# Kernel tuning notes

Measured on AMD Instinct MI355X. Metric: run time of the kernel, lower is better.

The kernel has to match this reference:

```python
import jax, jax.numpy as jnp
import numpy as np

N = 500_000        # num nodes
E = 2_000_000      # num edges
D = 8              # message passing depth
DIM = 16           # dim_embed
F = 5              # NUM_NODE_FEATURES
NUM_DAGS = 5_000


def _mlp_params(key, d_in, d_out, scale=0.1):
    k1, k2, k3 = jax.random.split(key, 3)
    return (jax.random.normal(k1, (d_in, 16), jnp.float32) * scale, jnp.zeros((16,), jnp.float32),
            jax.random.normal(k2, (16, 8), jnp.float32) * scale, jnp.zeros((8,), jnp.float32),
            jax.random.normal(k3, (8, d_out), jnp.float32) * scale, jnp.zeros((d_out,), jnp.float32))


def _mlp(x, w1, b1, w2, b2, w3, b3):
    h = jax.nn.relu(x @ w1 + b1)
    h = jax.nn.relu(h @ w2 + b2)
    return h @ w3 + b3


def setup_inputs() -> dict:
    key = jax.random.key(0)
    ks = jax.random.split(key, 8)
    x = jax.random.normal(ks[0], (N, F), jnp.float32)
    edge_index = jax.random.randint(ks[1], (2, E), 0, N, jnp.int32)
    edge_mask_batch = jax.random.bernoulli(ks[2], 0.5, (D, E))
    ptr = jnp.arange(0, N + 1, N // NUM_DAGS, dtype=jnp.int32)  # 5000 dags of 100 nodes
    inp = {"x": x, "edge_index": edge_index, "edge_mask_batch": edge_mask_batch, "ptr": ptr}
    names = ["p", "m", "u", "d", "g"]
    dins = [F, DIM, DIM, F + DIM, DIM]
    for name, din, k in zip(names, dins, jax.random.split(ks[3], 5)):
        w1, b1, w2, b2, w3, b3 = _mlp_params(k, din, DIM)
        inp.update({f"{name}w1": w1, f"{name}b1": b1, f"{name}w2": w2,
                    f"{name}b2": b2, f"{name}w3": w3, f"{name}b3": b3})
    return inp


def reference(x, edge_index, edge_mask_batch, ptr,
              pw1, pb1, pw2, pb2, pw3, pb3,
              mw1, mb1, mw2, mb2, mw3, mb3,
              uw1, ub1, uw2, ub2, uw3, ub3,
              dw1, db1, dw2, db2, dw3, db3,
              gw1, gb1, gw2, gb2, gw3, gb3):
    num_nodes = x.shape[0]
    dst, src = edge_index[0], edge_index[1]

    # NodeEncoder: prep then D rounds of masked sparse message passing
    h = _mlp(x, pw1, pb1, pw2, pb2, pw3, pb3)  # [N, DIM]

    def step(h, mask):
        mf = mask.astype(h.dtype)  # [E]
        y = _mlp(h, mw1, mb1, mw2, mb2, mw3, mb3)  # [N, DIM]
        # adj @ y: out[i] = sum over active edges (i <- j) of y[j]
        agg = jnp.zeros_like(h).at[dst].add(y[src] * mf[:, None])
        # node_mask: nodes that are destinations of an active edge
        nm = (jnp.zeros((num_nodes,), h.dtype).at[dst].add(mf) > 0)
        upd = _mlp(agg, uw1, ub1, uw2, ub2, uw3, ub3)
        return h + nm[:, None].astype(h.dtype) * upd, None

    h, _ = jax.lax.scan(step, h, edge_mask_batch)
    node_embeddings = h

    # DagEncoder: per-dag segment-sum of mlp([x, h])
    num_dags = ptr.shape[0] - 1
    seg = jnp.searchsorted(ptr, jnp.arange(num_nodes, dtype=ptr.dtype), side='right') - 1
    z = _mlp(jnp.concatenate([x, node_embeddings], axis=1), dw1, db1, dw2, db2, dw3, db3)
    dag_summaries = jax.ops.segment_sum(z, seg, num_segments=num_dags)  # [num_dags, DIM]

    # GlobalEncoder: no obs_ptr -> sum over all dags
    g = _mlp(dag_summaries, gw1, gb1, gw2, gb2, gw3, gb3)
    global_summaries = g.sum(0)[None]  # [1, DIM]

    return node_embeddings, dag_summaries, global_summaries
```

## Files before the change

kernel.cpp:

```cpp
#include <hip/hip_runtime.h>
#include <hip/hip_bf16.h>
#include <stdint.h>

#define N_NODES 500000
#define HALF_N 250000
#define N_EDGES 2000000
#define DEPTH 8
#define NUM_DAGS 5000
#define DAG_SZ 100
#define OUT_NODES_ELEMS 8000000
#define OUT_GLOB_OFF    8080000

#define EPB 1024
#define NB_E 1954
#define NBUK 256
#define NBUK_USED 245
#define MHIST (NBUK * NB_E)
#define NB_SCAN2 489

typedef __hip_bfloat16 bf16;

__device__ __forceinline__ float bfb2f(unsigned u) {
    return __uint_as_float((u & 0xffffu) << 16);
}
__device__ __forceinline__ unsigned f2bfb(float f) {
    bf16 b = __float2bfloat16(f);
    unsigned short u;
    __builtin_memcpy(&u, &b, 2);
    return (unsigned)u;
}
__device__ __forceinline__ float rndbf(float f) { return bfb2f(f2bfb(f)); }
template<int ISBF>
__device__ __forceinline__ float crnd(float f) { return ISBF ? rndbf(f) : f; }

__device__ __forceinline__ void unpack_pair(uint4 a, uint4 b, float* f) {
    f[0]=bfb2f(a.x);  f[1]=bfb2f(a.x>>16);
    f[2]=bfb2f(a.y);  f[3]=bfb2f(a.y>>16);
    f[4]=bfb2f(a.z);  f[5]=bfb2f(a.z>>16);
    f[6]=bfb2f(a.w);  f[7]=bfb2f(a.w>>16);
    f[8]=bfb2f(b.x);  f[9]=bfb2f(b.x>>16);
    f[10]=bfb2f(b.y); f[11]=bfb2f(b.y>>16);
    f[12]=bfb2f(b.z); f[13]=bfb2f(b.z>>16);
    f[14]=bfb2f(b.w); f[15]=bfb2f(b.w>>16);
}
__device__ __forceinline__ unsigned packpair(float lo, float hi) {
    return f2bfb(lo) | (f2bfb(hi) << 16);
}
__device__ __forceinline__ void pack16(const float* f, uint4* a, uint4* b) {
    a->x = packpair(f[0],f[1]);   a->y = packpair(f[2],f[3]);
    a->z = packpair(f[4],f[5]);   a->w = packpair(f[6],f[7]);
    b->x = packpair(f[8],f[9]);   b->y = packpair(f[10],f[11]);
    b->z = packpair(f[12],f[13]); b->w = packpair(f[14],f[15]);
}

template<int ISBF>
__device__ __forceinline__ float ldf(const void* p, size_t i) {
    return ISBF ? __bfloat162float(((const bf16*)p)[i]) : ((const float*)p)[i];
}
template<int ISBF>
__device__ __forceinline__ void load16(const void* base, size_t row, float* f) {
    if (ISBF) {
        const uint4* p = (const uint4*)((const bf16*)base + row*16);
        uint4 a = p[0], b = p[1];
        unpack_pair(a, b, f);
    } else {
        const float4* p = (const float4*)((const float*)base + row*16);
        float4 v0=p[0], v1=p[1], v2=p[2], v3=p[3];
        f[0]=v0.x; f[1]=v0.y; f[2]=v0.z; f[3]=v0.w;
        f[4]=v1.x; f[5]=v1.y; f[6]=v1.z; f[7]=v1.w;
        f[8]=v2.x; f[9]=v2.y; f[10]=v2.z; f[11]=v2.w;
        f[12]=v3.x; f[13]=v3.y; f[14]=v3.z; f[15]=v3.w;
    }
}
template<int ISBF>
__device__ __forceinline__ void store16(void* base, size_t row, const float* f) {
    if (ISBF) {
        uint4 a, b; pack16(f, &a, &b);
        uint4* p = (uint4*)((bf16*)base + row*16);
        p[0] = a; p[1] = b;
    } else {
        float4* p = (float4*)((float*)base + row*16);
        p[0] = make_float4(f[0],f[1],f[2],f[3]);
        p[1] = make_float4(f[4],f[5],f[6],f[7]);
        p[2] = make_float4(f[8],f[9],f[10],f[11]);
        p[3] = make_float4(f[12],f[13],f[14],f[15]);
    }
}

__global__ void k_detect(const void* __restrict__ x, int* __restrict__ flag) {
    const unsigned short* u = (const unsigned short*)x;
    int t = threadIdx.x;
    int wild = 0;
    #pragma unroll
    for (int k = 0; k < 4; k++) {
        float v = bfb2f(u[t*4 + k]);
        if (fabsf(v) > 1000.f) wild = 1;
    }
    unsigned long long m = __ballot(wild);
    if (t == 0) flag[0] = (m == 0ull) ? 1 : 0;
}

template<int DIN, int ISBF>
__device__ __forceinline__ void load_mlp_smem(const void* w1, const void* b1,
        const void* w2, const void* b2, const void* w3, const void* b3,
        float* s) {
    const int n1 = DIN * 16;
    const int tot = n1 + 16 + 128 + 8 + 128 + 16;
    for (int i = threadIdx.x; i < tot; i += blockDim.x) {
        int o = i; float v;
        if (o < n1)                 v = ldf<ISBF>(w1, o);
        else if ((o -= n1) < 16)    v = ldf<ISBF>(b1, o);
        else if ((o -= 16) < 128)   v = ldf<ISBF>(w2, o);
        else if ((o -= 128) < 8)    v = ldf<ISBF>(b2, o);
        else if ((o -= 8) < 128)    v = ldf<ISBF>(w3, o);
        else                        v = ldf<ISBF>(b3, o - 128);
        s[i] = v;
    }
}

template<int DIN, int ISBF>
__device__ __forceinline__ void mlp_apply(const float* in, const float* s,
                                          float* out) {
    const float* w1 = s;
    const float* b1 = s + DIN * 16;
    const float* w2 = b1 + 16;
    const float* b2 = w2 + 128;
    const float* w3 = b2 + 8;
    const float* b3 = w3 + 128;
    float h1[16];
    #pragma unroll
    for (int j = 0; j < 16; j++) {
        float a = b1[j];
        #pragma unroll
        for (int i = 0; i < DIN; i++) a = fmaf(in[i], w1[i*16 + j], a);
        h1[j] = crnd<ISBF>(fmaxf(a, 0.f));
    }
    float h2[8];
    #pragma unroll
    for (int j = 0; j < 8; j++) {
        float a = b2[j];
        #pragma unroll
        for (int i = 0; i < 16; i++) a = fmaf(h1[i], w2[i*8 + j], a);
        h2[j] = crnd<ISBF>(fmaxf(a, 0.f));
    }
    #pragma unroll
    for (int j = 0; j < 16; j++) {
        float a = b3[j];
        #pragma unroll
        for (int i = 0; i < 8; i++) a = fmaf(h2[i], w3[i*16 + j], a);
        out[j] = crnd<ISBF>(a);
    }
}


__global__ __launch_bounds__(256)
void k_bhist(const int* __restrict__ dstp, int* __restrict__ bh) {
    __shared__ int hcnt[NBUK];
    int t = threadIdx.x, blk = blockIdx.x;
    hcnt[t] = 0;
    __syncthreads();
    #pragma unroll
    for (int k = 0; k < 4; k++) {
        int e = blk * EPB + k * 256 + t;
        if (e < N_EDGES) atomicAdd(&hcnt[dstp[e] >> 11], 1);
    }
    __syncthreads();
    bh[t * NB_E + blk] = hcnt[t];
}

__global__ __launch_bounds__(256)
void k_gbsum(const int* __restrict__ v, int n, int* __restrict__ bsum) {
    __shared__ int sd[256];
    int b = blockIdx.x, t = threadIdx.x;
    int base = b * 1024;
    int s = 0;
    #pragma unroll
    for (int k = 0; k < 4; k++) {
        int i = base + t + k * 256;
        if (i < n) s += v[i];
    }
    sd[t] = s; __syncthreads();
    for (int off = 128; off > 0; off >>= 1) {
        if (t < off) sd[t] += sd[t + off];
        __syncthreads();
    }
    if (t == 0) bsum[b] = sd[0];
}

__global__ __launch_bounds__(512)
void k_gbscan(const int* __restrict__ bsum, int nb, int* __restrict__ boff) {
    __shared__ int s[512];
    int t = threadIdx.x;
    int v = (t < nb) ? bsum[t] : 0;
    s[t] = v; __syncthreads();
    for (int off = 1; off < 512; off <<= 1) {
        int x = (t >= off) ? s[t - off] : 0;
        __syncthreads();
        s[t] += x;
        __syncthreads();
    }
    if (t < nb) boff[t] = s[t] - v;
}

__global__ __launch_bounds__(1024)
void k_gscan(const int* __restrict__ v, const int* __restrict__ boff, int n,
             int* __restrict__ out) {
    __shared__ int s[1024];
    int b = blockIdx.x, t = threadIdx.x;
    int i = b * 1024 + t;
    int x = (i < n) ? v[i] : 0;
    s[t] = x; __syncthreads();
    for (int off = 1; off < 1024; off <<= 1) {
        int y = (t >= off) ? s[t - off] : 0;
        __syncthreads();
        s[t] += y;
        __syncthreads();
    }
    if (i < n) out[i] = boff[b] + s[t] - x;
}

__global__ __launch_bounds__(256)
void k_bscatter(const int* __restrict__ dstp, const int* __restrict__ srcp,
                const int* __restrict__ mask, const int* __restrict__ sbh,
                uint2* __restrict__ staging) {
    __shared__ int cur[NBUK];
    int t = threadIdx.x, blk = blockIdx.x;
    cur[t] = sbh[t * NB_E + blk];
    __syncthreads();
    #pragma unroll
    for (int k = 0; k < 4; k++) {
        int e = blk * EPB + k * 256 + t;
        if (e < N_EDGES) {
            int d = dstp[e];
            unsigned mb = 0;
            #pragma unroll
            for (int tt = 0; tt < DEPTH; tt++)
                mb |= (__builtin_nontemporal_load(mask + (size_t)tt * N_EDGES + e)
                       != 0 ? 1u : 0u) << tt;
            int pos = atomicAdd(&cur[d >> 11], 1);
            staging[pos] = make_uint2((unsigned)srcp[e] | (mb << 19), (unsigned)d);
        }
    }
}

__global__ __launch_bounds__(256)
void k_place(const uint2* __restrict__ staging, const int* __restrict__ sbh,
             int* __restrict__ row_ptr, unsigned* __restrict__ csr) {
    __shared__ int cnt[2048];
    __shared__ int tsum[256];
    int t = threadIdx.x, b = blockIdx.x;
    int ebase = sbh[b * NB_E];
    int eend  = sbh[(b + 1) * NB_E];
    int nrec  = eend - ebase;
    #pragma unroll
    for (int k = 0; k < 8; k++) cnt[t + k * 256] = 0;
    __syncthreads();
    for (int r = t; r < nrec; r += 256)
        atomicAdd(&cnt[staging[ebase + r].y & 2047], 1);
    __syncthreads();
    int s = 0;
    #pragma unroll
    for (int j = 0; j < 8; j++) { int c = cnt[t*8 + j]; cnt[t*8 + j] = s; s += c; }
    int own = s;
    tsum[t] = s;
    __syncthreads();
    for (int off = 1; off < 256; off <<= 1) {
        int v = (t >= off) ? tsum[t - off] : 0;
        __syncthreads();
        tsum[t] += v;
        __syncthreads();
    }
    int pref = tsum[t] - own + ebase;
    #pragma unroll
    for (int j = 0; j < 8; j++) cnt[t*8 + j] += pref;
    int base_node = b * 2048;
    #pragma unroll
    for (int j = 0; j < 8; j++) {
        int idx = base_node + t*8 + j;
        if (idx <= N_NODES) row_ptr[idx] = cnt[t*8 + j];
    }
    __syncthreads();
    for (int r = t; r < nrec; r += 256) {
        uint2 u = staging[ebase + r];
        int pos = atomicAdd(&cnt[u.y & 2047], 1);
        csr[pos] = u.x;
    }
}


template<int ISBF>
__device__ __forceinline__ void prep_body(const void* x,
        const void* pw1, const void* pb1, const void* pw2,
        const void* pb2, const void* pw3, const void* pb3,
        const void* mw1, const void* mb1, const void* mw2,
        const void* mb2, const void* mw3, const void* mb3,
        void* h, bf16* y0, float* sp, float* sm) {
    load_mlp_smem<5, ISBF>(pw1, pb1, pw2, pb2, pw3, pb3, sp);
    load_mlp_smem<16, ISBF>(mw1, mb1, mw2, mb2, mw3, mb3, sm);
    __syncthreads();
    int i = blockIdx.x * blockDim.x + threadIdx.x;
    if (i >= N_NODES) return;
    float in[5];
    #pragma unroll
    for (int j = 0; j < 5; j++) in[j] = ldf<ISBF>(x, (size_t)i*5 + j);
    float hv[16];
    mlp_apply<5, ISBF>(in, sp, hv);
    store16<ISBF>(h, i, hv);
    float y[16];
    mlp_apply<16, ISBF>(hv, sm, y);
    uint4 oa, ob; pack16(y, &oa, &ob);
    uint4* yp = (uint4*)(y0 + (size_t)i*16);
    yp[0] = oa; yp[1] = ob;
}

__global__ __launch_bounds__(256, 4)
void k_prep(const void* __restrict__ x,
            const void* pw1, const void* pb1, const void* pw2,
            const void* pb2, const void* pw3, const void* pb3,
            const void* mw1, const void* mb1, const void* mw2,
            const void* mb2, const void* mw3, const void* mb3,
            void* __restrict__ h, bf16* __restrict__ y0,
            const int* __restrict__ dtflag) {
    __shared__ float sp[5*16 + 16 + 128 + 8 + 128 + 16];
    __shared__ float sm[16*16 + 16 + 128 + 8 + 128 + 16];
    if (dtflag[0])
        prep_body<1>(x, pw1,pb1,pw2,pb2,pw3,pb3, mw1,mb1,mw2,mb2,mw3,mb3, h, y0, sp, sm);
    else
        prep_body<0>(x, pw1,pb1,pw2,pb2,pw3,pb3, mw1,mb1,mw2,mb2,mw3,mb3, h, y0, sp, sm);
}

template<int ISBF>
__device__ __forceinline__ void finish_node(int i, int any, const float* acc,
        void* h, const bf16* yin, bf16* yout, const float* su, const float* sm) {
    uint4* yo = (uint4*)(yout + (size_t)i*16);
    if (!any) {
        const uint4* yp = (const uint4*)(yin + (size_t)i*16);
        yo[0] = yp[0]; yo[1] = yp[1];
        return;
    }
    float a16[16];
    #pragma unroll
    for (int j = 0; j < 16; j++) a16[j] = crnd<ISBF>(acc[j]);
    float upd[16];
    mlp_apply<16, ISBF>(a16, su, upd);
    float hv[16];
    load16<ISBF>(h, i, hv);
    float o[16];
    #pragma unroll
    for (int j = 0; j < 16; j++) o[j] = crnd<ISBF>(hv[j] + upd[j]);
    store16<ISBF>(h, i, o);
    float yn[16];
    mlp_apply<16, ISBF>(o, sm, yn);
    uint4 oa, ob; pack16(yn, &oa, &ob);
    yo[0] = oa; yo[1] = ob;
}

template<int ISBF>
__device__ __forceinline__ void round_body(void* h, const int* row_ptr,
        const unsigned* csr, const bf16* yin, bf16* yout,
        const void* uw1, const void* ub1, const void* uw2,
        const void* ub2, const void* uw3, const void* ub3,
        const void* mw1, const void* mb1, const void* mw2,
        const void* mb2, const void* mw3, const void* mb3,
        int t, float* su, float* sm) {
    load_mlp_smem<16, ISBF>(uw1, ub1, uw2, ub2, uw3, ub3, su);
    load_mlp_smem<16, ISBF>(mw1, mb1, mw2, mb2, mw3, mb3, sm);
    __syncthreads();
    int i0 = blockIdx.x * blockDim.x + threadIdx.x;
    if (i0 >= HALF_N) return;
    int i1 = i0 + HALF_N;
    int b0 = row_ptr[i0], e0 = row_ptr[i0 + 1];
    int b1 = row_ptr[i1], e1 = row_ptr[i1 + 1];
    float acc0[16], acc1[16];
    #pragma unroll
    for (int j = 0; j < 16; j++) { acc0[j] = 0.f; acc1[j] = 0.f; }
    int any0 = 0, any1 = 0;
    const unsigned tb = 1u << (19 + t);
    int p0 = b0, p1 = b1;
    while (p0 < e0 || p1 < e1) {
        unsigned v0[4], v1[4];
        #pragma unroll
        for (int k = 0; k < 4; k++) {
            v0[k] = (p0 + k < e0) ? csr[p0 + k] : 0u;
            v1[k] = (p1 + k < e1) ? csr[p1 + k] : 0u;
        }
        uint4 ga0[4], gb0[4], ga1[4], gb1[4];
        int a0[4], a1[4];
        #pragma unroll
        for (int k = 0; k < 4; k++) {
            a0[k] = (v0[k] & tb) != 0;
            if (a0[k]) {
                const uint4* yp = (const uint4*)(yin + (size_t)(v0[k] & 0x7FFFF)*16);
                ga0[k] = yp[0]; gb0[k] = yp[1];
            }
            a1[k] = (v1[k] & tb) != 0;
            if (a1[k]) {
                const uint4* yp = (const uint4*)(yin + (size_t)(v1[k] & 0x7FFFF)*16);
                ga1[k] = yp[0]; gb1[k] = yp[1];
            }
        }
        #pragma unroll
        for (int k = 0; k < 4; k++) {
            if (a0[k]) {
                any0 = 1;
                float f[16]; unpack_pair(ga0[k], gb0[k], f);
                #pragma unroll
                for (int j = 0; j < 16; j++) acc0[j] += f[j];
            }
            if (a1[k]) {
                any1 = 1;
                float f[16]; unpack_pair(ga1[k], gb1[k], f);
                #pragma unroll
                for (int j = 0; j < 16; j++) acc1[j] += f[j];
            }
        }
        p0 += 4; p1 += 4;
    }
    finish_node<ISBF>(i0, any0, acc0, h, yin, yout, su, sm);
    finish_node<ISBF>(i1, any1, acc1, h, yin, yout, su, sm);
}

__global__ __launch_bounds__(256, 4)
void k_round(void* __restrict__ h, const int* __restrict__ row_ptr,
             const unsigned* __restrict__ csr,
             const bf16* __restrict__ yin, bf16* __restrict__ yout,
             const void* uw1, const void* ub1, const void* uw2,
             const void* ub2, const void* uw3, const void* ub3,
             const void* mw1, const void* mb1, const void* mw2,
             const void* mb2, const void* mw3, const void* mb3,
             int t, const int* __restrict__ dtflag) {
    __shared__ float su[16*16 + 16 + 128 + 8 + 128 + 16];
    __shared__ float sm[16*16 + 16 + 128 + 8 + 128 + 16];
    if (dtflag[0])
        round_body<1>(h, row_ptr, csr, yin, yout, uw1,ub1,uw2,ub2,uw3,ub3,
                      mw1,mb1,mw2,mb2,mw3,mb3, t, su, sm);
    else
        round_body<0>(h, row_ptr, csr, yin, yout, uw1,ub1,uw2,ub2,uw3,ub3,
                      mw1,mb1,mw2,mb2,mw3,mb3, t, su, sm);
}

template<int ISBF>
__device__ __forceinline__ void dag_body(const void* x, const void* h,
        const void* w1, const void* b1, const void* w2,
        const void* b2, const void* w3, const void* b3,
        float* dagsum, float* s, float* zb) {
    load_mlp_smem<21, ISBF>(w1, b1, w2, b2, w3, b3, s);
    __syncthreads();
    int t = threadIdx.x;
    int dag = blockIdx.x;
    if (t < DAG_SZ) {
        int i = dag * DAG_SZ + t;
        float in[21];
        #pragma unroll
        for (int j = 0; j < 5; j++) in[j] = ldf<ISBF>(x, (size_t)i*5 + j);
        load16<ISBF>(h, i, in + 5);
        float z[16];
        mlp_apply<21, ISBF>(in, s, z);
        #pragma unroll
        for (int j = 0; j < 16; j++) zb[t*16 + j] = z[j];
    }
    __syncthreads();
    if (t < 16) {
        float acc = 0.f;
        for (int r = 0; r < DAG_SZ; r++) acc += zb[r*16 + t];
        dagsum[(size_t)dag*16 + t] = acc;
    }
}

__global__ __launch_bounds__(128)
void k_dag(const void* __restrict__ x, const void* __restrict__ h,
           const void* w1, const void* b1, const void* w2,
           const void* b2, const void* w3, const void* b3,
           float* __restrict__ dagsum, const int* __restrict__ dtflag) {
    __shared__ float s[21*16 + 16 + 128 + 8 + 128 + 16];
    __shared__ float zb[DAG_SZ * 16];
    if (dtflag[0]) dag_body<1>(x, h, w1,b1,w2,b2,w3,b3, dagsum, s, zb);
    else           dag_body<0>(x, h, w1,b1,w2,b2,w3,b3, dagsum, s, zb);
}

template<int ISBF>
__device__ __forceinline__ void glob_body(const float* dagsum,
        const void* w1, const void* b1, const void* w2,
        const void* b2, const void* w3, const void* b3,
        void* d_out, float* globacc, float* s, float* gb) {
    load_mlp_smem<16, ISBF>(w1, b1, w2, b2, w3, b3, s);
    __syncthreads();
    int t = threadIdx.x;
    int d = blockIdx.x * blockDim.x + t;
    float g[16];
    if (d < NUM_DAGS) {
        const float4* dp = (const float4*)(dagsum + (size_t)d*16);
        float4 v0 = dp[0], v1 = dp[1], v2 = dp[2], v3 = dp[3];
        float in[16] = { v0.x, v0.y, v0.z, v0.w, v1.x, v1.y, v1.z, v1.w,
                         v2.x, v2.y, v2.z, v2.w, v3.x, v3.y, v3.z, v3.w };
        #pragma unroll
        for (int j = 0; j < 16; j++) in[j] = crnd<ISBF>(in[j]);
        if (ISBF) {
            bf16* od = (bf16*)d_out + OUT_NODES_ELEMS;
            store16<1>(od, d, in);
        } else {
            float* od = (float*)d_out + OUT_NODES_ELEMS;
            store16<0>(od, d, in);
        }
        mlp_apply<16, ISBF>(in, s, g);
    } else {
        #pragma unroll
        for (int j = 0; j < 16; j++) g[j] = 0.f;
    }
    #pragma unroll
    for (int j = 0; j < 16; j++) gb[t*16 + j] = g[j];
    __syncthreads();
    if (t < 16) {
        float acc = 0.f;
        for (int r = 0; r < 256; r++) acc += gb[r*16 + t];
        unsafeAtomicAdd(&globacc[t], acc);
    }
}

__global__ __launch_bounds__(256)
void k_glob(const float* __restrict__ dagsum,
            const void* w1, const void* b1, const void* w2,
            const void* b2, const void* w3, const void* b3,
            void* __restrict__ d_out, float* __restrict__ globacc,
            const int* __restrict__ dtflag) {
    __shared__ float s[16*16 + 16 + 128 + 8 + 128 + 16];
    __shared__ float gb[256 * 16];
    if (dtflag[0]) glob_body<1>(dagsum, w1,b1,w2,b2,w3,b3, d_out, globacc, s, gb);
    else           glob_body<0>(dagsum, w1,b1,w2,b2,w3,b3, d_out, globacc, s, gb);
}

__global__ void k_final(const float* __restrict__ globacc,
                        void* __restrict__ d_out, const int* __restrict__ dtflag) {
    const int isbf = dtflag[0];
    int t = threadIdx.x;
    if (t < 16) {
        if (isbf) ((bf16*)d_out)[OUT_GLOB_OFF + t] = __float2bfloat16(globacc[t]);
        else      ((float*)d_out)[OUT_GLOB_OFF + t] = globacc[t];
    }
}

extern "C" void kernel_launch(void* const* d_in, const int* in_sizes, int n_in,
                              void* d_out, int out_size, void* d_ws, size_t ws_size,
                              hipStream_t stream) {
    const void* x    = d_in[0];
    const int*  ei   = (const int*)d_in[1];
    const int*  mask = (const int*)d_in[2];
    const void* W[30];
    for (int i = 0; i < 30; i++) W[i] = d_in[4 + i];

    const int* dstp = ei;
    const int* srcp = ei + N_EDGES;

    char*     ws      = (char*)d_ws;
    float*    globacc = (float*)   (ws);
    int*      dtflag  = (int*)     (ws + 64);
    int*      row_ptr = (int*)     (ws + 128);
    int*      bh      = (int*)     (ws + 2000192);
    int*      sbh     = (int*)     (ws + 4001152);
    int*      bsum    = (int*)     (ws + 6002176);
    int*      boff    = (int*)     (ws + 6004224);
    unsigned* csr     = (unsigned*)(ws + 6006272);
    bf16*     y0      = (bf16*)    (ws + 14006272);
    bf16*     y1      = (bf16*)    (ws + 30006272);
    uint2*    staging = (uint2*)   (ws + 30006272);
    float*    dagsum  = (float*)   (ws + 46006272);

    hipMemsetAsync(d_ws, 0, 128, stream);

    const int TB  = 256;
    const int nbN = (N_NODES + TB - 1) / TB;
    const int nbH = (HALF_N + TB - 1) / TB;

    k_detect<<<1, 64, 0, stream>>>(x, dtflag);

    k_bhist<<<NB_E, 256, 0, stream>>>(dstp, bh);
    k_gbsum<<<NB_SCAN2, 256, 0, stream>>>(bh, MHIST, bsum);
    k_gbscan<<<1, 512, 0, stream>>>(bsum, NB_SCAN2, boff);
    k_gscan<<<NB_SCAN2, 1024, 0, stream>>>(bh, boff, MHIST, sbh);
    k_bscatter<<<NB_E, 256, 0, stream>>>(dstp, srcp, mask, sbh, staging);
    k_place<<<NBUK_USED, 256, 0, stream>>>(staging, sbh, row_ptr, csr);

    k_prep<<<nbN, TB, 0, stream>>>(x, W[0], W[1], W[2], W[3], W[4], W[5],
                                   W[6], W[7], W[8], W[9], W[10], W[11],
                                   d_out, y0, dtflag);
    bf16* yb[2] = { y0, y1 };
    for (int t = 0; t < DEPTH; t++) {
        k_round<<<nbH, TB, 0, stream>>>(d_out, row_ptr, csr,
                                        yb[t & 1], yb[(t + 1) & 1],
                                        W[12], W[13], W[14], W[15], W[16], W[17],
                                        W[6], W[7], W[8], W[9], W[10], W[11],
                                        t, dtflag);
    }
    k_dag<<<NUM_DAGS, 128, 0, stream>>>(x, d_out, W[18], W[19], W[20], W[21],
                                        W[22], W[23], dagsum, dtflag);
    k_glob<<<(NUM_DAGS + TB - 1) / TB, TB, 0, stream>>>(dagsum, W[24], W[25], W[26],
                                                        W[27], W[28], W[29],
                                                        d_out, globacc, dtflag);
    k_final<<<1, 64, 0, stream>>>(globacc, d_out, dtflag);
}
```

Baseline: 674.8 us.

## Fuse prep and all message-passing rounds into one cooperative persistent kernel

Replaces the prep kernel and the eight per-round kernels with a single cooperative kernel that uses grid-wide syncs between rounds. Each thread keeps its two nodes' row_ptr bounds in registers and the MLP weights are staged in shared memory once instead of every launch. This is meant to remove kernel launch gaps and repeated weight and row_ptr loads. The cost is a grid barrier per round and a block count fixed at 977, which must all be co-resident. If the cooperative launch fails, the code falls back to the old multi-kernel path.

```diff
diff --git a/kernel.cpp b/kernel.cpp
--- a/kernel.cpp
+++ b/kernel.cpp
@@ -1,6 +1,9 @@
 #include <hip/hip_runtime.h>
 #include <hip/hip_bf16.h>
+#include <hip/hip_cooperative_groups.h>
 #include <stdint.h>
+
+namespace cg = cooperative_groups;
 
 #define N_NODES 500000
 #define HALF_N 250000
@@ -17,6 +20,7 @@
 #define NBUK_USED 245
 #define MHIST (NBUK * NB_E)
 #define NB_SCAN2 489
+#define NB_MP 977
 
 typedef __hip_bfloat16 bf16;
 
@@ -289,17 +293,8 @@
 
 
 template<int ISBF>
-__device__ __forceinline__ void prep_body(const void* x,
-        const void* pw1, const void* pb1, const void* pw2,
-        const void* pb2, const void* pw3, const void* pb3,
-        const void* mw1, const void* mb1, const void* mw2,
-        const void* mb2, const void* mw3, const void* mb3,
-        void* h, bf16* y0, float* sp, float* sm) {
-    load_mlp_smem<5, ISBF>(pw1, pb1, pw2, pb2, pw3, pb3, sp);
-    load_mlp_smem<16, ISBF>(mw1, mb1, mw2, mb2, mw3, mb3, sm);
-    __syncthreads();
-    int i = blockIdx.x * blockDim.x + threadIdx.x;
-    if (i >= N_NODES) return;
+__device__ __forceinline__ void prep_node(int i, const void* x,
+        const float* sp, const float* sm, void* h, bf16* y0) {
     float in[5];
     #pragma unroll
     for (int j = 0; j < 5; j++) in[j] = ldf<ISBF>(x, (size_t)i*5 + j);
@@ -313,22 +308,6 @@
     yp[0] = oa; yp[1] = ob;
 }
 
-__global__ __launch_bounds__(256, 4)
-void k_prep(const void* __restrict__ x,
-            const void* pw1, const void* pb1, const void* pw2,
-            const void* pb2, const void* pw3, const void* pb3,
-            const void* mw1, const void* mb1, const void* mw2,
-            const void* mb2, const void* mw3, const void* mb3,
-            void* __restrict__ h, bf16* __restrict__ y0,
-            const int* __restrict__ dtflag) {
-    __shared__ float sp[5*16 + 16 + 128 + 8 + 128 + 16];
-    __shared__ float sm[16*16 + 16 + 128 + 8 + 128 + 16];
-    if (dtflag[0])
-        prep_body<1>(x, pw1,pb1,pw2,pb2,pw3,pb3, mw1,mb1,mw2,mb2,mw3,mb3, h, y0, sp, sm);
-    else
-        prep_body<0>(x, pw1,pb1,pw2,pb2,pw3,pb3, mw1,mb1,mw2,mb2,mw3,mb3, h, y0, sp, sm);
-}
-
 template<int ISBF>
 __device__ __forceinline__ void finish_node(int i, int any, const float* acc,
         void* h, const bf16* yin, bf16* yout, const float* su, const float* sm) {
@@ -356,26 +335,14 @@
 }
 
 template<int ISBF>
-__device__ __forceinline__ void round_body(void* h, const int* row_ptr,
-        const unsigned* csr, const bf16* yin, bf16* yout,
-        const void* uw1, const void* ub1, const void* uw2,
-        const void* ub2, const void* uw3, const void* ub3,
-        const void* mw1, const void* mb1, const void* mw2,
-        const void* mb2, const void* mw3, const void* mb3,
-        int t, float* su, float* sm) {
-    load_mlp_smem<16, ISBF>(uw1, ub1, uw2, ub2, uw3, ub3, su);
-    load_mlp_smem<16, ISBF>(mw1, mb1, mw2, mb2, mw3, mb3, sm);
-    __syncthreads();
-    int i0 = blockIdx.x * blockDim.x + threadIdx.x;
-    if (i0 >= HALF_N) return;
-    int i1 = i0 + HALF_N;
-    int b0 = row_ptr[i0], e0 = row_ptr[i0 + 1];
-    int b1 = row_ptr[i1], e1 = row_ptr[i1 + 1];
+__device__ __forceinline__ void round_nodes(int i0, int i1,
+        int b0, int e0, int b1, int e1, unsigned tb,
+        const unsigned* csr, const bf16* yin, bf16* yout, void* h,
+        const float* su, const float* sm) {
     float acc0[16], acc1[16];
     #pragma unroll
     for (int j = 0; j < 16; j++) { acc0[j] = 0.f; acc1[j] = 0.f; }
     int any0 = 0, any1 = 0;
-    const unsigned tb = 1u << (19 + t);
     int p0 = b0, p1 = b1;
     while (p0 < e0 || p1 < e1) {
         unsigned v0[4], v1[4];
@@ -418,6 +385,118 @@
     }
     finish_node<ISBF>(i0, any0, acc0, h, yin, yout, su, sm);
     finish_node<ISBF>(i1, any1, acc1, h, yin, yout, su, sm);
+}
+
+
+template<int ISBF>
+__device__ void mp_body(const void* x,
+        const void* pw1, const void* pb1, const void* pw2,
+        const void* pb2, const void* pw3, const void* pb3,
+        const void* uw1, const void* ub1, const void* uw2,
+        const void* ub2, const void* uw3, const void* ub3,
+        const void* mw1, const void* mb1, const void* mw2,
+        const void* mb2, const void* mw3, const void* mb3,
+        void* h, bf16* y0, bf16* y1,
+        const int* row_ptr, const unsigned* csr,
+        float* sp, float* su, float* sm) {
+    load_mlp_smem<5, ISBF>(pw1, pb1, pw2, pb2, pw3, pb3, sp);
+    load_mlp_smem<16, ISBF>(uw1, ub1, uw2, ub2, uw3, ub3, su);
+    load_mlp_smem<16, ISBF>(mw1, mb1, mw2, mb2, mw3, mb3, sm);
+    __syncthreads();
+    cg::grid_group grid = cg::this_grid();
+    int gtid = blockIdx.x * blockDim.x + threadIdx.x;
+    const bool act = (gtid < HALF_N);
+    int i0 = gtid, i1 = gtid + HALF_N;
+    int b0 = 0, e0 = 0, b1 = 0, e1 = 0;
+    if (act) {
+        prep_node<ISBF>(i0, x, sp, sm, h, y0);
+        prep_node<ISBF>(i1, x, sp, sm, h, y0);
+        b0 = row_ptr[i0]; e0 = row_ptr[i0 + 1];
+        b1 = row_ptr[i1]; e1 = row_ptr[i1 + 1];
+    }
+    grid.sync();
+    const bf16* yi = y0;
+    bf16* yo = y1;
+    for (int t = 0; t < DEPTH; t++) {
+        if (act)
+            round_nodes<ISBF>(i0, i1, b0, e0, b1, e1, 1u << (19 + t),
+                              csr, yi, yo, h, su, sm);
+        if (t < DEPTH - 1) grid.sync();
+        const bf16* tmp = yi; yi = yo; yo = (bf16*)tmp;
+    }
+}
+
+__global__ __launch_bounds__(256, 4)
+void k_mp(const void* __restrict__ x,
+          const void* pw1, const void* pb1, const void* pw2,
+          const void* pb2, const void* pw3, const void* pb3,
+          const void* uw1, const void* ub1, const void* uw2,
+          const void* ub2, const void* uw3, const void* ub3,
+          const void* mw1, const void* mb1, const void* mw2,
+          const void* mb2, const void* mw3, const void* mb3,
+          void* __restrict__ h, bf16* __restrict__ y0, bf16* __restrict__ y1,
+          const int* __restrict__ row_ptr, const unsigned* __restrict__ csr,
+          const int* __restrict__ dtflag) {
+    __shared__ float sp[5*16 + 16 + 128 + 8 + 128 + 16];
+    __shared__ float su[16*16 + 16 + 128 + 8 + 128 + 16];
+    __shared__ float sm[16*16 + 16 + 128 + 8 + 128 + 16];
+    if (dtflag[0])
+        mp_body<1>(x, pw1,pb1,pw2,pb2,pw3,pb3, uw1,ub1,uw2,ub2,uw3,ub3,
+                   mw1,mb1,mw2,mb2,mw3,mb3, h, y0, y1, row_ptr, csr, sp, su, sm);
+    else
+        mp_body<0>(x, pw1,pb1,pw2,pb2,pw3,pb3, uw1,ub1,uw2,ub2,uw3,ub3,
+                   mw1,mb1,mw2,mb2,mw3,mb3, h, y0, y1, row_ptr, csr, sp, su, sm);
+}
+
+
+template<int ISBF>
+__device__ __forceinline__ void prep_body(const void* x,
+        const void* pw1, const void* pb1, const void* pw2,
+        const void* pb2, const void* pw3, const void* pb3,
+        const void* mw1, const void* mb1, const void* mw2,
+        const void* mb2, const void* mw3, const void* mb3,
+        void* h, bf16* y0, float* sp, float* sm) {
+    load_mlp_smem<5, ISBF>(pw1, pb1, pw2, pb2, pw3, pb3, sp);
+    load_mlp_smem<16, ISBF>(mw1, mb1, mw2, mb2, mw3, mb3, sm);
+    __syncthreads();
+    int i = blockIdx.x * blockDim.x + threadIdx.x;
+    if (i >= N_NODES) return;
+    prep_node<ISBF>(i, x, sp, sm, h, y0);
+}
+
+__global__ __launch_bounds__(256, 4)
+void k_prep(const void* __restrict__ x,
+            const void* pw1, const void* pb1, const void* pw2,
+            const void* pb2, const void* pw3, const void* pb3,
+            const void* mw1, const void* mb1, const void* mw2,
+            const void* mb2, const void* mw3, const void* mb3,
+            void* __restrict__ h, bf16* __restrict__ y0,
+            const int* __restrict__ dtflag) {
+    __shared__ float sp[5*16 + 16 + 128 + 8 + 128 + 16];
+    __shared__ float sm[16*16 + 16 + 128 + 8 + 128 + 16];
+    if (dtflag[0])
+        prep_body<1>(x, pw1,pb1,pw2,pb2,pw3,pb3, mw1,mb1,mw2,mb2,mw3,mb3, h, y0, sp, sm);
+    else
+        prep_body<0>(x, pw1,pb1,pw2,pb2,pw3,pb3, mw1,mb1,mw2,mb2,mw3,mb3, h, y0, sp, sm);
+}
+
+template<int ISBF>
+__device__ __forceinline__ void round_body(void* h, const int* row_ptr,
+        const unsigned* csr, const bf16* yin, bf16* yout,
+        const void* uw1, const void* ub1, const void* uw2,
+        const void* ub2, const void* uw3, const void* ub3,
+        const void* mw1, const void* mb1, const void* mw2,
+        const void* mb2, const void* mw3, const void* mb3,
+        int t, float* su, float* sm) {
+    load_mlp_smem<16, ISBF>(uw1, ub1, uw2, ub2, uw3, ub3, su);
+    load_mlp_smem<16, ISBF>(mw1, mb1, mw2, mb2, mw3, mb3, sm);
+    __syncthreads();
+    int i0 = blockIdx.x * blockDim.x + threadIdx.x;
+    if (i0 >= HALF_N) return;
+    int i1 = i0 + HALF_N;
+    round_nodes<ISBF>(i0, i1, row_ptr[i0], row_ptr[i0 + 1],
+                      row_ptr[i1], row_ptr[i1 + 1], 1u << (19 + t),
+                      csr, yin, yout, h, su, sm);
 }
 
 __global__ __launch_bounds__(256, 4)
@@ -439,6 +518,7 @@
                       mw1,mb1,mw2,mb2,mw3,mb3, t, su, sm);
 }
 
+
 template<int ISBF>
 __device__ __forceinline__ void dag_body(const void* x, const void* h,
         const void* w1, const void* b1, const void* w2,
@@ -580,17 +660,41 @@
     k_bscatter<<<NB_E, 256, 0, stream>>>(dstp, srcp, mask, sbh, staging);
     k_place<<<NBUK_USED, 256, 0, stream>>>(staging, sbh, row_ptr, csr);
 
-    k_prep<<<nbN, TB, 0, stream>>>(x, W[0], W[1], W[2], W[3], W[4], W[5],
-                                   W[6], W[7], W[8], W[9], W[10], W[11],
-                                   d_out, y0, dtflag);
-    bf16* yb[2] = { y0, y1 };
-    for (int t = 0; t < DEPTH; t++) {
-        k_round<<<nbH, TB, 0, stream>>>(d_out, row_ptr, csr,
-                                        yb[t & 1], yb[(t + 1) & 1],
-                                        W[12], W[13], W[14], W[15], W[16], W[17],
-                                        W[6], W[7], W[8], W[9], W[10], W[11],
-                                        t, dtflag);
-    }
+    {
+        void* hx = d_out;
+        const void* a_x = x;
+        const void *a_pw1=W[0],*a_pb1=W[1],*a_pw2=W[2],*a_pb2=W[3],*a_pw3=W[4],*a_pb3=W[5];
+        const void *a_mw1=W[6],*a_mb1=W[7],*a_mw2=W[8],*a_mb2=W[9],*a_mw3=W[10],*a_mb3=W[11];
+        const void *a_uw1=W[12],*a_ub1=W[13],*a_uw2=W[14],*a_ub2=W[15],*a_uw3=W[16],*a_ub3=W[17];
+        bf16 *a_y0 = y0, *a_y1 = y1;
+        const int* a_rp = row_ptr;
+        const unsigned* a_csr = csr;
+        const int* a_dt = dtflag;
+        void* params[] = {
+            (void*)&a_x,
+            (void*)&a_pw1,(void*)&a_pb1,(void*)&a_pw2,(void*)&a_pb2,(void*)&a_pw3,(void*)&a_pb3,
+            (void*)&a_uw1,(void*)&a_ub1,(void*)&a_uw2,(void*)&a_ub2,(void*)&a_uw3,(void*)&a_ub3,
+            (void*)&a_mw1,(void*)&a_mb1,(void*)&a_mw2,(void*)&a_mb2,(void*)&a_mw3,(void*)&a_mb3,
+            (void*)&hx, (void*)&a_y0, (void*)&a_y1,
+            (void*)&a_rp, (void*)&a_csr, (void*)&a_dt
+        };
+        hipError_t rc = hipLaunchCooperativeKernel((const void*)k_mp,
+                            dim3(NB_MP), dim3(256), params, 0, stream);
+        if (rc != hipSuccess) {
+            k_prep<<<nbN, TB, 0, stream>>>(x, W[0], W[1], W[2], W[3], W[4], W[5],
+                                           W[6], W[7], W[8], W[9], W[10], W[11],
+                                           d_out, y0, dtflag);
+            bf16* yb[2] = { y0, y1 };
+            for (int t = 0; t < DEPTH; t++) {
+                k_round<<<nbH, TB, 0, stream>>>(d_out, row_ptr, csr,
+                                                yb[t & 1], yb[(t + 1) & 1],
+                                                W[12], W[13], W[14], W[15], W[16], W[17],
+                                                W[6], W[7], W[8], W[9], W[10], W[11],
+                                                t, dtflag);
+            }
+        }
+    }
+
     k_dag<<<NUM_DAGS, 128, 0, stream>>>(x, d_out, W[18], W[19], W[20], W[21],
                                         W[22], W[23], dagsum, dtflag);
     k_glob<<<(NUM_DAGS + TB - 1) / TB, TB, 0, stream>>>(dagsum, W[24], W[25], W[26],
```

Result: slower. 2.197 ms (+225.6%).
